# Performance work log

Hardware: AMD Instinct MI355X
Metric: run time of the kernel (lower is better)

Reference implementation:

```python
import jax, jax.numpy as jnp
import numpy as np

N_NODES = 100000
N_EDGES = 1600000
N_GRAPHS = 512


def _graph_conv(x, W, b, src, dst, n_nodes):
    """DGL GraphConv, norm='both': D_in^-1/2 (A (D_out^-1/2 x)) W + b.
    Weight is applied on the smaller-dim side (same math, less memory)."""
    ones = jnp.ones(src.shape[0], dtype=x.dtype)
    deg_out = jnp.clip(jax.ops.segment_sum(ones, src, num_segments=n_nodes), 1.0)
    deg_in = jnp.clip(jax.ops.segment_sum(ones, dst, num_segments=n_nodes), 1.0)
    h = x * (deg_out ** -0.5)[:, None]
    if W.shape[0] > W.shape[1]:  # reduce feature dim before the SpMM
        h = h @ W
        h = jax.ops.segment_sum(h[src], dst, num_segments=n_nodes)
    else:
        h = jax.ops.segment_sum(h[src], dst, num_segments=n_nodes)
        h = h @ W
    return h * (deg_in ** -0.5)[:, None] + b


def setup_inputs() -> dict:
    key = jax.random.key(0)
    ks = jax.random.split(key, 16)
    x = jax.random.normal(ks[0], (N_NODES, 128), dtype=jnp.float32)
    src = jax.random.randint(ks[1], (N_EDGES,), 0, N_NODES, dtype=jnp.int32)
    dst = jax.random.randint(ks[2], (N_EDGES,), 0, N_NODES, dtype=jnp.int32)
    graph_ids = jnp.sort(jax.random.randint(ks[3], (N_NODES,), 0, N_GRAPHS, dtype=jnp.int32))
    s = 0.05
    return {
        "x": x, "src": src, "dst": dst, "graph_ids": graph_ids,
        "W1": jax.random.normal(ks[4], (128, 256), jnp.float32) * s,
        "b1": jnp.zeros((256,), jnp.float32),
        "W2": jax.random.normal(ks[5], (256, 64), jnp.float32) * s,
        "b2": jnp.zeros((64,), jnp.float32),
        "Wc1": jax.random.normal(ks[6], (64, 18), jnp.float32) * s,
        "bc1": jnp.zeros((18,), jnp.float32),
        "Wc2": jax.random.normal(ks[7], (18, 12), jnp.float32) * s,
        "bc2": jnp.zeros((12,), jnp.float32),
        "Wc3": jax.random.normal(ks[8], (12, 6), jnp.float32) * s,
        "bc3": jnp.zeros((6,), jnp.float32),
        "Wc4": jax.random.normal(ks[9], (6, 2), jnp.float32) * s,
        "bc4": jnp.zeros((2,), jnp.float32),
    }


def reference(x, src, dst, graph_ids, W1, b1, W2, b2, Wc1, bc1, Wc2, bc2, Wc3, bc3, Wc4, bc4):
    n = x.shape[0]
    h = jax.nn.relu(_graph_conv(x, W1, b1, src, dst, n))
    h = jax.nn.relu(_graph_conv(h, W2, b2, src, dst, n))
    # dgl.mean_nodes: per-graph mean over nodes
    sums = jax.ops.segment_sum(h, graph_ids, num_segments=N_GRAPHS)
    cnts = jnp.clip(jax.ops.segment_sum(jnp.ones(n, h.dtype), graph_ids, num_segments=N_GRAPHS), 1.0)
    hg = sums / cnts[:, None]
    # classifier: 4 stacked Linear layers, no activations (faithful to source)
    hg = hg @ Wc1 + bc1
    hg = hg @ Wc2 + bc2
    hg = hg @ Wc3 + bc3
    return hg @ Wc4 + bc4
```

## Files before the change

### kernel.cpp

```cpp
#include <hip/hip_runtime.h>
#include <cstdint>
#include <cstddef>

#define NGRAPHS 512

static inline size_t align_up(size_t x, size_t a){ return (x + a - 1) & ~(a - 1); }

__device__ __forceinline__ unsigned short f2bf(float f){
  unsigned int u = __float_as_uint(f);
  u += 0x7FFFu + ((u >> 16) & 1u);
  return (unsigned short)(u >> 16);
}
__device__ __forceinline__ float bflo(unsigned int u){ return __uint_as_float(u << 16); }
__device__ __forceinline__ float bfhi(unsigned int u){ return __uint_as_float(u & 0xffff0000u); }
__device__ __forceinline__ unsigned int pack2(float a, float b){
  return (unsigned)f2bf(a) | ((unsigned)f2bf(b) << 16);
}

typedef __attribute__((ext_vector_type(8))) short bf16x8;
typedef __attribute__((ext_vector_type(4))) float f32x4;

__global__ __launch_bounds__(256) void k_partcount(const int* __restrict__ src, const int* __restrict__ dst,
                                                   int* __restrict__ cntS, int* __restrict__ cntD, int n_edges, int NBLK,
                                                   const float* __restrict__ W1, unsigned short* __restrict__ Wt1,
                                                   const float* __restrict__ W2, unsigned short* __restrict__ Wt2,
                                                   const int* __restrict__ gids, int* __restrict__ gb, int n_nodes){
  __shared__ int cs[256], cd[256];
  if (blockIdx.x >= NBLK){
    long long u = (long long)(blockIdx.x - NBLK) * 256 + threadIdx.x;
    if (u < 128 * 256){
      int k = (int)(u / 256), n = (int)(u % 256);
      Wt1[(size_t)n * 128 + k] = f2bf(W1[u]);
      return;
    }
    u -= 128 * 256;
    if (u < 256 * 64){
      int k = (int)(u / 64), n = (int)(u % 64);
      Wt2[(size_t)n * 256 + k] = f2bf(W2[u]);
      return;
    }
    u -= 256 * 64;
    if (u < n_nodes){
      int i = (int)u;
      int g  = gids[i];
      int gp = (i > 0) ? gids[i - 1] : -1;
      for (int q = gp + 1; q <= g; ++q) gb[q] = i;
      if (i == n_nodes - 1)
        for (int q = g + 1; q <= NGRAPHS; ++q) gb[q] = n_nodes;
    }
    return;
  }
  int tid = threadIdx.x;
  cs[tid] = 0; cd[tid] = 0;
  __syncthreads();
  int e0 = blockIdx.x * 4096;
  int e1 = min(e0 + 4096, n_edges);
  for (int e = e0 + tid; e < e1; e += 256){
    atomicAdd(&cs[src[e] >> 9], 1);
    atomicAdd(&cd[dst[e] >> 9], 1);
  }
  __syncthreads();
  cntS[blockIdx.x * 256 + tid] = cs[tid];
  cntD[blockIdx.x * 256 + tid] = cd[tid];
}

__global__ __launch_bounds__(256) void k_colscan(int* __restrict__ cntS, int* __restrict__ cntD,
                                                 int* __restrict__ totS, int* __restrict__ totD,
                                                 int nblk, int NB){
  int col = blockIdx.x;
  int* cnt; int* tot; int k;
  if (col < NB){ cnt = cntS; tot = totS; k = col; }
  else         { cnt = cntD; tot = totD; k = col - NB; }
  __shared__ int tsum[256];
  int tid = threadIdx.x;
  int i0 = 2 * tid, i1 = 2 * tid + 1;
  int a = (i0 < nblk) ? cnt[i0 * 256 + k] : 0;
  int b = (i1 < nblk) ? cnt[i1 * 256 + k] : 0;
  int s = a + b;
  tsum[tid] = s;
  __syncthreads();
  for (int off = 1; off < 256; off <<= 1){
    int t = (tid >= off) ? tsum[tid - off] : 0;
    __syncthreads();
    tsum[tid] += t;
    __syncthreads();
  }
  int pre = tsum[tid] - s;
  if (i0 < nblk) cnt[i0 * 256 + k] = pre;
  if (i1 < nblk) cnt[i1 * 256 + k] = pre + a;
  if (tid == 255) tot[k] = tsum[255];
}

__global__ __launch_bounds__(256) void k_scatter_det(const int* __restrict__ src, const int* __restrict__ dst,
                                                     const int* __restrict__ cntS, const int* __restrict__ cntD,
                                                     const int* __restrict__ totS, const int* __restrict__ totD,
                                                     int* __restrict__ baseS, int* __restrict__ baseD,
                                                     int2* __restrict__ pairD, int* __restrict__ srcS,
                                                     int n_edges, int NB){
  __shared__ int s1[256], s2[256];
  __shared__ int gbS[256], gbD[256], lsS[256], lsD[256], lcS[256], lcD[256];
  __shared__ int2 ebuf[4096];
  __shared__ int sbuf[4096];
  int tid = threadIdx.x;
  int b = blockIdx.x;
  int v1 = (tid < NB) ? totS[tid] : 0;
  int v2 = (tid < NB) ? totD[tid] : 0;
  s1[tid] = v1; s2[tid] = v2;
  __syncthreads();
  for (int off = 1; off < 256; off <<= 1){
    int t1 = (tid >= off) ? s1[tid - off] : 0;
    int t2 = (tid >= off) ? s2[tid - off] : 0;
    __syncthreads();
    s1[tid] += t1; s2[tid] += t2;
    __syncthreads();
  }
  int bS = s1[tid] - v1, bD = s2[tid] - v2;
  if (b == 0 && tid < NB){ baseS[tid] = bS; baseD[tid] = bD; }
  gbS[tid] = bS + cntS[b * 256 + tid];
  gbD[tid] = bD + cntD[b * 256 + tid];
  __syncthreads();
  int e0 = b * 4096, e1 = min(e0 + 4096, n_edges);
  int ne = e1 - e0;
  s1[tid] = 0; s2[tid] = 0;
  __syncthreads();
  for (int e = e0 + tid; e < e1; e += 256){
    atomicAdd(&s1[src[e] >> 9], 1);
    atomicAdd(&s2[dst[e] >> 9], 1);
  }
  __syncthreads();
  int hv1 = s1[tid], hv2 = s2[tid];
  __syncthreads();
  s1[tid] = hv1; s2[tid] = hv2;
  __syncthreads();
  for (int off = 1; off < 256; off <<= 1){
    int t1 = (tid >= off) ? s1[tid - off] : 0;
    int t2 = (tid >= off) ? s2[tid - off] : 0;
    __syncthreads();
    s1[tid] += t1; s2[tid] += t2;
    __syncthreads();
  }
  lsS[tid] = s1[tid] - hv1; lcS[tid] = lsS[tid];
  lsD[tid] = s2[tid] - hv2; lcD[tid] = lsD[tid];
  __syncthreads();
  for (int e = e0 + tid; e < e1; e += 256){
    int sv = src[e], d = dst[e];
    int lp = atomicAdd(&lcD[d >> 9], 1);
    ebuf[lp] = make_int2(sv, d);
    int sp = atomicAdd(&lcS[sv >> 9], 1);
    sbuf[sp] = sv;
  }
  __syncthreads();
  for (int i = tid; i < ne; i += 256){
    int2 e = ebuf[i];
    int kd = e.y >> 9;
    pairD[gbD[kd] + i - lsD[kd]] = e;
    int sv = sbuf[i];
    int ks = sv >> 9;
    srcS[gbS[ks] + i - lsS[ks]] = sv;
  }
}

__global__ __launch_bounds__(256) void k_bucket_build(const int2* __restrict__ pairD, const int* __restrict__ baseD,
                                                      const int* __restrict__ srcS, const int* __restrict__ baseS,
                                                      int* __restrict__ offs, float* __restrict__ din_s,
                                                      float* __restrict__ dout_s, int* __restrict__ csr_src,
                                                      int NB, int n, int n_edges){
  __shared__ int cnt[512], cur[512];
  __shared__ int tsum[256];
  int tid = threadIdx.x;
  int bb = blockIdx.x;
  bool dstSide = bb < NB;
  int b = dstSide ? bb : bb - NB;
  int node0 = b << 9;
  int nn = min(512, n - node0);
  for (int i = tid; i < 512; i += 256) cnt[i] = 0;
  __syncthreads();
  if (dstSide){
    int jd0 = baseD[b], jd1 = (b + 1 < NB) ? baseD[b + 1] : n_edges;
    for (int j = jd0 + tid; j < jd1; j += 256) atomicAdd(&cnt[pairD[j].y - node0], 1);
    __syncthreads();
    int a0 = cnt[2 * tid], a1 = cnt[2 * tid + 1];
    int s = a0 + a1;
    tsum[tid] = s;
    __syncthreads();
    for (int off = 1; off < 256; off <<= 1){
      int t = (tid >= off) ? tsum[tid - off] : 0;
      __syncthreads();
      tsum[tid] += t;
      __syncthreads();
    }
    int pre = tsum[tid] - s + jd0;
    cur[2 * tid]     = pre;
    cur[2 * tid + 1] = pre + a0;
    __syncthreads();
    for (int i = tid; i < nn; i += 256){
      offs[node0 + i]  = cur[i];
      din_s[node0 + i] = 1.0f / sqrtf((float)max(cnt[i], 1));
    }
    if (b == NB - 1 && tid == 0) offs[n] = n_edges;
    __syncthreads();
    for (int j = jd0 + tid; j < jd1; j += 256){
      int2 e = pairD[j];
      int p = atomicAdd(&cur[e.y - node0], 1);
      csr_src[p] = e.x;
    }
  } else {
    int js0 = baseS[b], js1 = (b + 1 < NB) ? baseS[b + 1] : n_edges;
    for (int j = js0 + tid; j < js1; j += 256) atomicAdd(&cnt[srcS[j] - node0], 1);
    __syncthreads();
    for (int i = tid; i < nn; i += 256)
      dout_s[node0 + i] = 1.0f / sqrtf((float)max(cnt[i], 1));
  }
}

__global__ __launch_bounds__(256) void k_prep2(const float* __restrict__ x,
                                               const float* __restrict__ dout_s,
                                               unsigned int* __restrict__ xb, long long total4){
  long long t = (long long)blockIdx.x * 256 + threadIdx.x;
  if (t >= total4) return;
  float4 v = ((const float4*)x)[t];
  float s = dout_s[t >> 5];
  xb[t * 2 + 0] = pack2(v.x * s, v.y * s);
  xb[t * 2 + 1] = pack2(v.z * s, v.w * s);
}

__global__ __launch_bounds__(256) void k_spmm1(const unsigned int* __restrict__ xb,
    const int* __restrict__ offs, const int* __restrict__ csr_src,
    unsigned int* __restrict__ aggb, int n_nodes){
  int node = __builtin_amdgcn_readfirstlane((int)((blockIdx.x * 256u + threadIdx.x) >> 6));
  if (node >= n_nodes) return;
  int lane = threadIdx.x & 63;
  int j0 = offs[node], j1 = offs[node + 1];
  float ax = 0.f, ay = 0.f;
  int j = j0;
  for (; j + 4 <= j1; j += 4){
    int s0 = csr_src[j + 0];
    int s1 = csr_src[j + 1];
    int s2 = csr_src[j + 2];
    int s3 = csr_src[j + 3];
    unsigned v0 = xb[(size_t)s0 * 64 + lane];
    unsigned v1 = xb[(size_t)s1 * 64 + lane];
    unsigned v2 = xb[(size_t)s2 * 64 + lane];
    unsigned v3 = xb[(size_t)s3 * 64 + lane];
    ax += bflo(v0) + bflo(v1) + bflo(v2) + bflo(v3);
    ay += bfhi(v0) + bfhi(v1) + bfhi(v2) + bfhi(v3);
  }
  for (; j < j1; ++j){
    unsigned v = xb[(size_t)csr_src[j] * 64 + lane];
    ax += bflo(v);
    ay += bfhi(v);
  }
  aggb[(size_t)node * 64 + lane] = pack2(ax, ay);
}

__global__ __launch_bounds__(256) void k_gemm1(const unsigned short* __restrict__ A,
    const unsigned short* __restrict__ Bt, unsigned short* __restrict__ C,
    int M, const float* __restrict__ din, const float* __restrict__ dout,
    const float* __restrict__ bias){
  constexpr int LDA = 136;
  __shared__ __align__(16) unsigned short As[128 * LDA];
  __shared__ __align__(16) unsigned short Bs[64 * LDA];
  int tid = threadIdx.x;
  int bm0 = blockIdx.x * 128;
  int wid = tid >> 6, lane = tid & 63;
  int wm = wid * 32;
  int quad = lane >> 4, l16 = lane & 15;

  uint4 areg[8];
#pragma unroll
  for (int it = 0; it < 8; ++it){
    int i = tid + it * 256;
    int m = i >> 4, c = i & 15;
    int gr = bm0 + m;
    areg[it] = (gr < M) ? *(const uint4*)(A + (size_t)gr * 128 + c * 8) : make_uint4(0u, 0u, 0u, 0u);
  }
  uint4 breg[4];
#pragma unroll
  for (int it = 0; it < 4; ++it){
    int i = tid + it * 256;
    int n = i >> 4, c = i & 15;
    breg[it] = *(const uint4*)(Bt + (size_t)n * 128 + c * 8);
  }
#pragma unroll
  for (int it = 0; it < 8; ++it){
    int i = tid + it * 256;
    int m = i >> 4, c = i & 15;
    *(uint4*)&As[m * LDA + c * 8] = areg[it];
  }
#pragma unroll
  for (int it = 0; it < 4; ++it){
    int i = tid + it * 256;
    int n = i >> 4, c = i & 15;
    *(uint4*)&Bs[n * LDA + c * 8] = breg[it];
  }
  float rsv[2][4], rs2v[2][4];
#pragma unroll
  for (int t = 0; t < 2; ++t)
#pragma unroll
    for (int r = 0; r < 4; ++r){
      int gr = bm0 + wm + t * 16 + quad * 4 + r;
      rsv[t][r]  = (gr < M) ? din[gr]  : 0.f;
      rs2v[t][r] = (gr < M) ? dout[gr] : 0.f;
    }
  __syncthreads();

  for (int nt = 0; nt < 4; ++nt){
    if (nt < 3){
#pragma unroll
      for (int it = 0; it < 4; ++it){
        int i = tid + it * 256;
        int n = i >> 4, c = i & 15;
        breg[it] = *(const uint4*)(Bt + (size_t)((nt + 1) * 64 + n) * 128 + c * 8);
      }
    }
    f32x4 acc[2][4];
#pragma unroll
    for (int t = 0; t < 2; ++t)
#pragma unroll
      for (int u = 0; u < 4; ++u) acc[t][u] = f32x4{0.f, 0.f, 0.f, 0.f};
#pragma unroll
    for (int ks = 0; ks < 4; ++ks){
      bf16x8 af[2], bfr[4];
#pragma unroll
      for (int t = 0; t < 2; ++t)
        af[t] = *(const bf16x8*)&As[(wm + t * 16 + l16) * LDA + ks * 32 + quad * 8];
#pragma unroll
      for (int u = 0; u < 4; ++u)
        bfr[u] = *(const bf16x8*)&Bs[(u * 16 + l16) * LDA + ks * 32 + quad * 8];
#pragma unroll
      for (int t = 0; t < 2; ++t)
#pragma unroll
        for (int u = 0; u < 4; ++u)
          acc[t][u] = __builtin_amdgcn_mfma_f32_16x16x32_bf16(af[t], bfr[u], acc[t][u], 0, 0, 0);
    }
    float bv[4];
#pragma unroll
    for (int u = 0; u < 4; ++u) bv[u] = bias[nt * 64 + u * 16 + l16];
#pragma unroll
    for (int t = 0; t < 2; ++t){
#pragma unroll
      for (int r = 0; r < 4; ++r){
        int gr = bm0 + wm + t * 16 + quad * 4 + r;
        if (gr < M){
#pragma unroll
          for (int u = 0; u < 4; ++u){
            float cv = fmaxf(fmaf(acc[t][u][r], rsv[t][r], bv[u]), 0.f) * rs2v[t][r];
            C[(size_t)gr * 256 + nt * 64 + u * 16 + l16] = f2bf(cv);
          }
        }
      }
    }
    if (nt < 3){
      __syncthreads();
#pragma unroll
      for (int it = 0; it < 4; ++it){
        int i = tid + it * 256;
        int n = i >> 4, c = i & 15;
        *(uint4*)&Bs[n * LDA + c * 8] = breg[it];
      }
      __syncthreads();
    }
  }
}

#define SCHUNK 4
__global__ __launch_bounds__(256) void k_spmm2_fused(const unsigned short* __restrict__ t2,
    const int* __restrict__ offs, const int* __restrict__ csr_src,
    const float* __restrict__ din_s, const float* __restrict__ b2,
    const int* __restrict__ gb, float* __restrict__ sums){
  __shared__ float bs[64];
  int tid = threadIdx.x;
  int g = blockIdx.x & (NGRAPHS - 1);
  int chunk = blockIdx.x >> 9;
  int wW = __builtin_amdgcn_readfirstlane(chunk * 4 + (tid >> 6));
  int lane = tid & 63, half = lane >> 5, l = lane & 31;
  if (tid < 64) bs[tid] = 0.f;
  __syncthreads();
  int g0 = gb[g], g1 = gb[g + 1];
  const unsigned int* tp = (const unsigned int*)t2;
  float2 bb = ((const float2*)b2)[l];
  float gxs = 0.f, gys = 0.f;
  for (int node = g0 + wW; node < g1; node += 16){
    int j0 = offs[node], j1 = offs[node + 1];
    float ax = 0.f, ay = 0.f;
    int j = j0;
    for (; j + 2 <= j1; j += 2){
      int s0 = csr_src[j], s1 = csr_src[j + 1];
      int ss = half ? s1 : s0;
      unsigned v = tp[(size_t)ss * 32 + l];
      ax += bflo(v);
      ay += bfhi(v);
    }
    if (j < j1 && half == 0){
      unsigned v = tp[(size_t)csr_src[j] * 32 + l];
      ax += bflo(v);
      ay += bfhi(v);
    }
    ax += __shfl_xor(ax, 32);
    ay += __shfl_xor(ay, 32);
    float ds = din_s[node];
    gxs += fmaxf(fmaf(ax, ds, bb.x), 0.f);
    gys += fmaxf(fmaf(ay, ds, bb.y), 0.f);
  }
  if (half == 0){
    atomicAdd(&bs[2 * l], gxs);
    atomicAdd(&bs[2 * l + 1], gys);
  }
  __syncthreads();
  if (tid < 64) atomicAdd(&sums[(size_t)g * 64 + tid], bs[tid]);
}

template<bool C_BF16, bool EPI, bool EPI2>
__global__ __launch_bounds__(256) void gemm_mfma(
    const unsigned short* __restrict__ A, const unsigned short* __restrict__ Bt, void* __restrict__ Cp,
    int M, int N, int K,
    const float* __restrict__ rowScaleC, const float* __restrict__ rowScaleC2,
    const float* __restrict__ bias){
  constexpr int BM = 128, BN = 64, BK = 32, LDA = 40;
  __shared__ __align__(16) unsigned short As[2][BM * LDA];
  __shared__ __align__(16) unsigned short Bs[2][BN * LDA];
  int tid = threadIdx.x;
  int bm0 = blockIdx.x * BM;
  int bn0 = blockIdx.y * BN;
  int wid = tid >> 6, lane = tid & 63;
  int wm = (wid >> 1) * 64, wn = (wid & 1) * 32;
  int quad = lane >> 4, l16 = lane & 15;
  f32x4 acc[4][2];
#pragma unroll
  for (int t = 0; t < 4; ++t)
#pragma unroll
    for (int u = 0; u < 2; ++u) acc[t][u] = f32x4{0.f, 0.f, 0.f, 0.f};

  uint2 ar[4], br[2];
  auto preload = [&](int kk){
#pragma unroll
    for (int it = 0; it < 4; ++it){
      int i = tid + it * 256;
      int m = i >> 3, c = i & 7;
      int gr = bm0 + m;
      ar[it] = (gr < M) ? *(const uint2*)(A + (size_t)gr * K + kk + c * 4) : make_uint2(0u, 0u);
    }
#pragma unroll
    for (int it = 0; it < 2; ++it){
      int i = tid + it * 256;
      int n = i >> 3, c = i & 7;
      br[it] = *(const uint2*)(Bt + (size_t)(bn0 + n) * K + kk + c * 4);
    }
  };
  auto commit = [&](int buf){
#pragma unroll
    for (int it = 0; it < 4; ++it){
      int i = tid + it * 256;
      int m = i >> 3, c = i & 7;
      *(uint2*)&As[buf][m * LDA + c * 4] = ar[it];
    }
#pragma unroll
    for (int it = 0; it < 2; ++it){
      int i = tid + it * 256;
      int n = i >> 3, c = i & 7;
      *(uint2*)&Bs[buf][n * LDA + c * 4] = br[it];
    }
  };

  preload(0);
  commit(0);
  __syncthreads();
  int nk = K / BK;
  for (int kb = 0; kb < nk; ++kb){
    int cur = kb & 1;
    if (kb + 1 < nk) preload((kb + 1) * BK);
    bf16x8 af[4], bfr[2];
#pragma unroll
    for (int t = 0; t < 4; ++t)
      af[t] = *(const bf16x8*)&As[cur][(wm + t * 16 + l16) * LDA + quad * 8];
#pragma unroll
    for (int u = 0; u < 2; ++u)
      bfr[u] = *(const bf16x8*)&Bs[cur][(wn + u * 16 + l16) * LDA + quad * 8];
#pragma unroll
    for (int t = 0; t < 4; ++t)
#pragma unroll
      for (int u = 0; u < 2; ++u)
        acc[t][u] = __builtin_amdgcn_mfma_f32_16x16x32_bf16(af[t], bfr[u], acc[t][u], 0, 0, 0);
    if (kb + 1 < nk){
      commit(cur ^ 1);
      __syncthreads();
    }
  }
  float bv[2] = {0.f, 0.f};
  if constexpr (EPI){ bv[0] = bias[bn0 + wn + l16]; bv[1] = bias[bn0 + wn + 16 + l16]; }
#pragma unroll
  for (int t = 0; t < 4; ++t){
#pragma unroll
    for (int r = 0; r < 4; ++r){
      int gr = bm0 + wm + t * 16 + quad * 4 + r;
      if (gr < M){
        float rs = 1.f, rs2 = 1.f;
        if constexpr (EPI)  rs  = rowScaleC[gr];
        if constexpr (EPI2) rs2 = rowScaleC2[gr];
#pragma unroll
        for (int u = 0; u < 2; ++u){
          int gc = bn0 + wn + u * 16 + l16;
          float cv = acc[t][u][r];
          if constexpr (EPI)  cv = fmaxf(fmaf(cv, rs, bv[u]), 0.f);
          if constexpr (EPI2) cv *= rs2;
          if constexpr (C_BF16) ((unsigned short*)Cp)[(size_t)gr * N + gc] = f2bf(cv);
          else                  ((float*)Cp)[(size_t)gr * N + gc] = cv;
        }
      }
    }
  }
}

__global__ __launch_bounds__(256) void k_classifier(const float* __restrict__ sums, const int* __restrict__ gb,
    const float* __restrict__ Wc1, const float* __restrict__ bc1,
    const float* __restrict__ Wc2, const float* __restrict__ bc2,
    const float* __restrict__ Wc3, const float* __restrict__ bc3,
    const float* __restrict__ Wc4, const float* __restrict__ bc4,
    float* __restrict__ out){
  __shared__ float w1[64 * 18], w2[18 * 12], w3[12 * 6], w4[6 * 2];
  __shared__ float B1[18], B2[12], B3[6], B4[2];
  int tid = threadIdx.x;
  for (int i = tid; i < 64 * 18; i += 256) w1[i] = Wc1[i];
  for (int i = tid; i < 18 * 12; i += 256) w2[i] = Wc2[i];
  for (int i = tid; i < 12 * 6;  i += 256) w3[i] = Wc3[i];
  for (int i = tid; i < 6 * 2;   i += 256) w4[i] = Wc4[i];
  if (tid < 18) B1[tid] = bc1[tid];
  if (tid < 12) B2[tid] = bc2[tid];
  if (tid < 6)  B3[tid] = bc3[tid];
  if (tid < 2)  B4[tid] = bc4[tid];
  __syncthreads();
  int g = blockIdx.x * 256 + tid;
  float cnt = fmaxf((float)(gb[g + 1] - gb[g]), 1.0f);
  float h[64];
#pragma unroll
  for (int f = 0; f < 64; ++f) h[f] = sums[(size_t)g * 64 + f] / cnt;
  float t1[18];
#pragma unroll
  for (int j = 0; j < 18; ++j){
    float s = B1[j];
    for (int f = 0; f < 64; ++f) s = fmaf(h[f], w1[f * 18 + j], s);
    t1[j] = s;
  }
  float t2[12];
#pragma unroll
  for (int j = 0; j < 12; ++j){
    float s = B2[j];
    for (int f = 0; f < 18; ++f) s = fmaf(t1[f], w2[f * 12 + j], s);
    t2[j] = s;
  }
  float t3[6];
#pragma unroll
  for (int j = 0; j < 6; ++j){
    float s = B3[j];
    for (int f = 0; f < 12; ++f) s = fmaf(t2[f], w3[f * 6 + j], s);
    t3[j] = s;
  }
#pragma unroll
  for (int j = 0; j < 2; ++j){
    float s = B4[j];
    for (int f = 0; f < 6; ++f) s = fmaf(t3[f], w4[f * 2 + j], s);
    out[(size_t)g * 2 + j] = s;
  }
}

extern "C" void kernel_launch(void* const* d_in, const int* in_sizes, int n_in,
                              void* d_out, int out_size, void* d_ws, size_t ws_size,
                              hipStream_t stream){
  const float* x   = (const float*)d_in[0];
  const int*   src = (const int*)d_in[1];
  const int*   dst = (const int*)d_in[2];
  const int*   gid = (const int*)d_in[3];
  const float* W1  = (const float*)d_in[4];
  const float* b1  = (const float*)d_in[5];
  const float* W2  = (const float*)d_in[6];
  const float* b2  = (const float*)d_in[7];
  const float* Wc1 = (const float*)d_in[8];
  const float* bc1 = (const float*)d_in[9];
  const float* Wc2 = (const float*)d_in[10];
  const float* bc2 = (const float*)d_in[11];
  const float* Wc3 = (const float*)d_in[12];
  const float* bc3 = (const float*)d_in[13];
  const float* Wc4 = (const float*)d_in[14];
  const float* bc4 = (const float*)d_in[15];
  float* out = (float*)d_out;

  const int n_nodes = in_sizes[3];
  const int n_edges = in_sizes[1];
  const int F1 = 256, F2 = 64;
  const int NB   = (n_nodes + 511) >> 9;
  const int NBLK = (n_edges + 4095) / 4096;

  char* w = (char*)d_ws;
  size_t o = 0;
  auto alloc = [&](size_t bytes) -> char* {
    char* p = w + o;
    o = align_up(o + bytes, 256);
    return p;
  };
  float* sums      = (float*)alloc((size_t)NGRAPHS * F2 * 4);
  int*   gb        = (int*)  alloc((size_t)(NGRAPHS + 1) * 4);
  int*   cntS      = (int*)  alloc((size_t)NBLK * 256 * 4);
  int*   cntD      = (int*)  alloc((size_t)NBLK * 256 * 4);
  int*   totS      = (int*)  alloc((size_t)256 * 4);
  int*   totD      = (int*)  alloc((size_t)256 * 4);
  int*   baseS     = (int*)  alloc((size_t)256 * 4);
  int*   baseD     = (int*)  alloc((size_t)256 * 4);
  float* dout_s    = (float*)alloc((size_t)n_nodes * 4);
  float* din_s     = (float*)alloc((size_t)n_nodes * 4);
  int*   offs      = (int*)  alloc((size_t)(n_nodes + 1) * 4);
  int*   csr_src   = (int*)  alloc((size_t)n_edges * 4);
  unsigned short* Wt1 = (unsigned short*)alloc((size_t)256 * 128 * 2);
  unsigned short* Wt2 = (unsigned short*)alloc((size_t)64 * 256 * 2);
  unsigned int*   xb  = (unsigned int*)  alloc((size_t)n_nodes * 128 * 2);
  unsigned short* aggb= (unsigned short*)alloc((size_t)n_nodes * 128 * 2);
  unsigned short* h1b = (unsigned short*)alloc((size_t)n_nodes * F1 * 2);
  int2*  pairD = (int2*)aggb;
  int*   srcS  = (int*)((char*)aggb + (size_t)n_edges * 8);
  unsigned short* t2b = aggb;

  hipMemsetAsync(sums, 0, (size_t)NGRAPHS * F2 * 4, stream);

  {
    long long miscTotal = 128 * 256 + 256 * 64 + n_nodes;
    int miscBlocks = (int)((miscTotal + 255) / 256);
    k_partcount<<<NBLK + miscBlocks, 256, 0, stream>>>(src, dst, cntS, cntD, n_edges, NBLK,
                                                       W1, Wt1, W2, Wt2, gid, gb, n_nodes);
  }
  k_colscan     <<<2 * NB, 256, 0, stream>>>(cntS, cntD, totS, totD, NBLK, NB);
  k_scatter_det <<<NBLK, 256, 0, stream>>>(src, dst, cntS, cntD, totS, totD, baseS, baseD, pairD, srcS, n_edges, NB);
  k_bucket_build<<<2 * NB, 256, 0, stream>>>(pairD, baseD, srcS, baseS, offs, din_s, dout_s, csr_src,
                                             NB, n_nodes, n_edges);

  {
    long long total4 = (long long)n_nodes * 32;
    k_prep2<<<(int)((total4 + 255) / 256), 256, 0, stream>>>(x, dout_s, xb, total4);
  }

  int gx = (n_nodes + 127) / 128;
  {
    long long threads = (long long)n_nodes * 64;
    k_spmm1<<<(int)((threads + 255) / 256), 256, 0, stream>>>(xb, offs, csr_src, (unsigned int*)aggb, n_nodes);
    k_gemm1<<<gx, 256, 0, stream>>>(aggb, Wt1, h1b, n_nodes, din_s, dout_s, b1);
  }
  {
    gemm_mfma<true, false, false><<<dim3(gx, 1), 256, 0, stream>>>(
        h1b, Wt2, t2b, n_nodes, F2, F1, nullptr, nullptr, nullptr);
    k_spmm2_fused<<<NGRAPHS * SCHUNK, 256, 0, stream>>>(t2b, offs, csr_src, din_s, b2, gb, sums);
  }
  k_classifier<<<NGRAPHS / 256, 256, 0, stream>>>(sums, gb, Wc1, bc1, Wc2, bc2, Wc3, bc3, Wc4, bc4, out);
}
```

Baseline: 357.0 us.

## Fuse layer-2 weight GEMM into layer-1 GEMM via shared-memory H tile

The layer-1 GEMM epilogue now writes each 64-column slice of the ReLU'd hidden activations into a shared-memory tile. That tile is immediately multiplied by the matching slice of W2, read directly from global memory, and the results accumulate into a 128x64 output per block. This removes the global write and re-read of the 100000x256 bf16 hidden tensor, and drops the separate second GEMM launch. In exchange it adds two extra barriers per column tile, more shared memory and registers, and uncached global loads of W2 inside the loop.

Result: faster. 345.2 us (-3.3%).

```diff
diff --git a/kernel.cpp b/kernel.cpp
--- a/kernel.cpp
+++ b/kernel.cpp
@@ -253,13 +253,16 @@
   aggb[(size_t)node * 64 + lane] = pack2(ax, ay);
 }
 
-__global__ __launch_bounds__(256) void k_gemm1(const unsigned short* __restrict__ A,
-    const unsigned short* __restrict__ Bt, unsigned short* __restrict__ C,
+__global__ __launch_bounds__(256) void k_gemm12(const unsigned short* __restrict__ A,
+    const unsigned short* __restrict__ Bt, const unsigned short* __restrict__ Wt2,
+    unsigned short* __restrict__ T2,
     int M, const float* __restrict__ din, const float* __restrict__ dout,
     const float* __restrict__ bias){
   constexpr int LDA = 136;
+  constexpr int LDH = 72;
   __shared__ __align__(16) unsigned short As[128 * LDA];
   __shared__ __align__(16) unsigned short Bs[64 * LDA];
+  __shared__ __align__(16) unsigned short Hs[128 * LDH];
   int tid = threadIdx.x;
   int bm0 = blockIdx.x * 128;
   int wid = tid >> 6, lane = tid & 63;
@@ -302,6 +305,11 @@
       rsv[t][r]  = (gr < M) ? din[gr]  : 0.f;
       rs2v[t][r] = (gr < M) ? dout[gr] : 0.f;
     }
+  f32x4 tacc[2][4];
+#pragma unroll
+  for (int t = 0; t < 2; ++t)
+#pragma unroll
+    for (int u = 0; u < 4; ++u) tacc[t][u] = f32x4{0.f, 0.f, 0.f, 0.f};
   __syncthreads();
 
   for (int nt = 0; nt < 4; ++nt){
@@ -337,21 +345,34 @@
 #pragma unroll
     for (int u = 0; u < 4; ++u) bv[u] = bias[nt * 64 + u * 16 + l16];
 #pragma unroll
-    for (int t = 0; t < 2; ++t){
+    for (int t = 0; t < 2; ++t)
 #pragma unroll
       for (int r = 0; r < 4; ++r){
-        int gr = bm0 + wm + t * 16 + quad * 4 + r;
-        if (gr < M){
-#pragma unroll
-          for (int u = 0; u < 4; ++u){
-            float cv = fmaxf(fmaf(acc[t][u][r], rsv[t][r], bv[u]), 0.f) * rs2v[t][r];
-            C[(size_t)gr * 256 + nt * 64 + u * 16 + l16] = f2bf(cv);
-          }
+        int row = wm + t * 16 + quad * 4 + r;
+#pragma unroll
+        for (int u = 0; u < 4; ++u){
+          float cv = fmaxf(fmaf(acc[t][u][r], rsv[t][r], bv[u]), 0.f) * rs2v[t][r];
+          Hs[row * LDH + u * 16 + l16] = f2bf(cv);
         }
       }
-    }
+    __syncthreads();
+#pragma unroll
+    for (int ks2 = 0; ks2 < 2; ++ks2){
+      bf16x8 haf[2], wbf[4];
+#pragma unroll
+      for (int t = 0; t < 2; ++t)
+        haf[t] = *(const bf16x8*)&Hs[(wm + t * 16 + l16) * LDH + ks2 * 32 + quad * 8];
+#pragma unroll
+      for (int u = 0; u < 4; ++u)
+        wbf[u] = *(const bf16x8*)(Wt2 + (size_t)(u * 16 + l16) * 256 + nt * 64 + ks2 * 32 + quad * 8);
+#pragma unroll
+      for (int t = 0; t < 2; ++t)
+#pragma unroll
+        for (int u = 0; u < 4; ++u)
+          tacc[t][u] = __builtin_amdgcn_mfma_f32_16x16x32_bf16(haf[t], wbf[u], tacc[t][u], 0, 0, 0);
+    }
+    __syncthreads();
     if (nt < 3){
-      __syncthreads();
 #pragma unroll
       for (int it = 0; it < 4; ++it){
         int i = tid + it * 256;
@@ -361,6 +382,17 @@
       __syncthreads();
     }
   }
+#pragma unroll
+  for (int t = 0; t < 2; ++t)
+#pragma unroll
+    for (int r = 0; r < 4; ++r){
+      int gr = bm0 + wm + t * 16 + quad * 4 + r;
+      if (gr < M){
+#pragma unroll
+        for (int u = 0; u < 4; ++u)
+          T2[(size_t)gr * 64 + u * 16 + l16] = f2bf(tacc[t][u][r]);
+      }
+    }
 }
 
 #define SCHUNK 4
@@ -408,107 +440,6 @@
   }
   __syncthreads();
   if (tid < 64) atomicAdd(&sums[(size_t)g * 64 + tid], bs[tid]);
-}
-
-template<bool C_BF16, bool EPI, bool EPI2>
-__global__ __launch_bounds__(256) void gemm_mfma(
-    const unsigned short* __restrict__ A, const unsigned short* __restrict__ Bt, void* __restrict__ Cp,
-    int M, int N, int K,
-    const float* __restrict__ rowScaleC, const float* __restrict__ rowScaleC2,
-    const float* __restrict__ bias){
-  constexpr int BM = 128, BN = 64, BK = 32, LDA = 40;
-  __shared__ __align__(16) unsigned short As[2][BM * LDA];
-  __shared__ __align__(16) unsigned short Bs[2][BN * LDA];
-  int tid = threadIdx.x;
-  int bm0 = blockIdx.x * BM;
-  int bn0 = blockIdx.y * BN;
-  int wid = tid >> 6, lane = tid & 63;
-  int wm = (wid >> 1) * 64, wn = (wid & 1) * 32;
-  int quad = lane >> 4, l16 = lane & 15;
-  f32x4 acc[4][2];
-#pragma unroll
-  for (int t = 0; t < 4; ++t)
-#pragma unroll
-    for (int u = 0; u < 2; ++u) acc[t][u] = f32x4{0.f, 0.f, 0.f, 0.f};
-
-  uint2 ar[4], br[2];
-  auto preload = [&](int kk){
-#pragma unroll
-    for (int it = 0; it < 4; ++it){
-      int i = tid + it * 256;
-      int m = i >> 3, c = i & 7;
-      int gr = bm0 + m;
-      ar[it] = (gr < M) ? *(const uint2*)(A + (size_t)gr * K + kk + c * 4) : make_uint2(0u, 0u);
-    }
-#pragma unroll
-    for (int it = 0; it < 2; ++it){
-      int i = tid + it * 256;
-      int n = i >> 3, c = i & 7;
-      br[it] = *(const uint2*)(Bt + (size_t)(bn0 + n) * K + kk + c * 4);
-    }
-  };
-  auto commit = [&](int buf){
-#pragma unroll
-    for (int it = 0; it < 4; ++it){
-      int i = tid + it * 256;
-      int m = i >> 3, c = i & 7;
-      *(uint2*)&As[buf][m * LDA + c * 4] = ar[it];
-    }
-#pragma unroll
-    for (int it = 0; it < 2; ++it){
-      int i = tid + it * 256;
-      int n = i >> 3, c = i & 7;
-      *(uint2*)&Bs[buf][n * LDA + c * 4] = br[it];
-    }
-  };
-
-  preload(0);
-  commit(0);
-  __syncthreads();
-  int nk = K / BK;
-  for (int kb = 0; kb < nk; ++kb){
-    int cur = kb & 1;
-    if (kb + 1 < nk) preload((kb + 1) * BK);
-    bf16x8 af[4], bfr[2];
-#pragma unroll
-    for (int t = 0; t < 4; ++t)
-      af[t] = *(const bf16x8*)&As[cur][(wm + t * 16 + l16) * LDA + quad * 8];
-#pragma unroll
-    for (int u = 0; u < 2; ++u)
-      bfr[u] = *(const bf16x8*)&Bs[cur][(wn + u * 16 + l16) * LDA + quad * 8];
-#pragma unroll
-    for (int t = 0; t < 4; ++t)
-#pragma unroll
-      for (int u = 0; u < 2; ++u)
-        acc[t][u] = __builtin_amdgcn_mfma_f32_16x16x32_bf16(af[t], bfr[u], acc[t][u], 0, 0, 0);
-    if (kb + 1 < nk){
-      commit(cur ^ 1);
-      __syncthreads();
-    }
-  }
-  float bv[2] = {0.f, 0.f};
-  if constexpr (EPI){ bv[0] = bias[bn0 + wn + l16]; bv[1] = bias[bn0 + wn + 16 + l16]; }
-#pragma unroll
-  for (int t = 0; t < 4; ++t){
-#pragma unroll
-    for (int r = 0; r < 4; ++r){
-      int gr = bm0 + wm + t * 16 + quad * 4 + r;
-      if (gr < M){
-        float rs = 1.f, rs2 = 1.f;
-        if constexpr (EPI)  rs  = rowScaleC[gr];
-        if constexpr (EPI2) rs2 = rowScaleC2[gr];
-#pragma unroll
-        for (int u = 0; u < 2; ++u){
-          int gc = bn0 + wn + u * 16 + l16;
-          float cv = acc[t][u][r];
-          if constexpr (EPI)  cv = fmaxf(fmaf(cv, rs, bv[u]), 0.f);
-          if constexpr (EPI2) cv *= rs2;
-          if constexpr (C_BF16) ((unsigned short*)Cp)[(size_t)gr * N + gc] = f2bf(cv);
-          else                  ((float*)Cp)[(size_t)gr * N + gc] = cv;
-        }
-      }
-    }
-  }
 }
 
 __global__ __launch_bounds__(256) void k_classifier(const float* __restrict__ sums, const int* __restrict__ gb,
@@ -616,7 +547,7 @@
   unsigned short* h1b = (unsigned short*)alloc((size_t)n_nodes * F1 * 2);
   int2*  pairD = (int2*)aggb;
   int*   srcS  = (int*)((char*)aggb + (size_t)n_edges * 8);
-  unsigned short* t2b = aggb;
+  unsigned short* t2b = h1b;
 
   hipMemsetAsync(sums, 0, (size_t)NGRAPHS * F2 * 4, stream);
 
@@ -640,12 +571,8 @@
   {
     long long threads = (long long)n_nodes * 64;
     k_spmm1<<<(int)((threads + 255) / 256), 256, 0, stream>>>(xb, offs, csr_src, (unsigned int*)aggb, n_nodes);
-    k_gemm1<<<gx, 256, 0, stream>>>(aggb, Wt1, h1b, n_nodes, din_s, dout_s, b1);
-  }
-  {
-    gemm_mfma<true, false, false><<<dim3(gx, 1), 256, 0, stream>>>(
-        h1b, Wt2, t2b, n_nodes, F2, F1, nullptr, nullptr, nullptr);
-    k_spmm2_fused<<<NGRAPHS * SCHUNK, 256, 0, stream>>>(t2b, offs, csr_src, din_s, b2, gb, sums);
-  }
+    k_gemm12<<<gx, 256, 0, stream>>>(aggb, Wt1, Wt2, t2b, n_nodes, din_s, dout_s, b1);
+  }
+  k_spmm2_fused<<<NGRAPHS * SCHUNK, 256, 0, stream>>>(t2b, offs, csr_src, din_s, b2, gb, sums);
   k_classifier<<<NGRAPHS / 256, 256, 0, stream>>>(sums, gb, Wc1, bc1, Wc2, bc2, Wc3, bc3, Wc4, bc4, out);
 }
```
